# Optimization experiments

Hardware: AMD Instinct MI355X
Metric: run time of the kernel (lower is better)

## Reference

```python
import jax, jax.numpy as jnp
import numpy as np

N = 4096          # nodes
IN_DIM = 256
OUT_DIM = 128
EDGE_DIM = 64
N_SAMPLE = 128
N_EDGES = 65536   # undirected edges (edge ids 1..N_EDGES; id 0 = no edge)
ALPHA = 0.2       # leaky-relu negative slope


def _glorot(key, shape):
    fan_in, fan_out = shape[0], shape[-1]
    scale = 1.414 * np.sqrt(2.0 / (fan_in + fan_out))
    return jax.random.normal(key, shape, jnp.float32) * scale


def setup_inputs() -> dict:
    rng = np.random.default_rng(0)
    # sample unique undirected edges (i < j); np.unique sorts lexicographically,
    # which matches torch's row-major e_index.nonzero() ordering, so assigning
    # sequential ids 1..n here makes edges == arange(1, n+1) in the update step.
    ii = rng.integers(0, N, size=3 * N_EDGES)
    jj = rng.integers(0, N, size=3 * N_EDGES)
    lo, hi = np.minimum(ii, jj), np.maximum(ii, jj)
    ok = lo < hi
    pairs = np.unique(np.stack([lo[ok], hi[ok]], axis=1), axis=0)[:N_EDGES]
    n = pairs.shape[0]
    ids = np.arange(1, n + 1, dtype=np.int32)
    e_index = np.zeros((N, N), np.int32)
    e_index[pairs[:, 0], pairs[:, 1]] = ids
    e_index[pairs[:, 1], pairs[:, 0]] = ids
    # per-node neighbor sampling with replacement (hoisted from torch forward)
    neigh = np.empty((N, N_SAMPLE), np.int32)
    for v in range(N):
        nz = np.nonzero(e_index[v])[0]
        neigh[v] = v if nz.size == 0 else rng.choice(nz, N_SAMPLE)

    key = jax.random.key(0)
    ks = jax.random.split(key, 8)
    return {
        "features": jax.random.normal(ks[0], (N, IN_DIM), jnp.float32),
        "e_index": jnp.asarray(e_index),
        "neigh": jnp.asarray(neigh),
        "to_update": jnp.asarray(pairs.astype(np.int32)),
        "emb": jax.random.normal(ks[1], (n + 1, EDGE_DIM), jnp.float32),
        "W": _glorot(ks[2], (IN_DIM, OUT_DIM)),
        "W2": _glorot(ks[3], (OUT_DIM, EDGE_DIM)),
        "W3": _glorot(ks[4], (EDGE_DIM, EDGE_DIM)),
        "B": _glorot(ks[5], (1, EDGE_DIM)),
        "a": _glorot(ks[6], (2 * OUT_DIM + EDGE_DIM, 1)),
    }


def reference(features, e_index, neigh, to_update, emb, W, W2, W3, B, a):
    x = features @ W                                        # [N, OUT]
    xn = x[neigh]                                           # [N, S, OUT] gather
    eid = jnp.take_along_axis(e_index, neigh, axis=1)       # [N, S] edge ids
    en = emb[eid]                                           # [N, S, ED] gather
    a_input = jnp.concatenate(
        [jnp.broadcast_to(x[:, None, :], xn.shape), xn, en], axis=2
    )                                                       # [N, S, 2*OUT+ED]
    e = jax.nn.leaky_relu((a_input @ a)[..., 0], ALPHA)     # [N, S]
    att = jax.nn.softmax(e, axis=1)                         # dropout = id (eval)
    h_prime = jnp.einsum('ns,nsd->nd', att, xn)             # [N, OUT]
    output = jax.nn.elu(h_prime + x)
    # edge update: (output[i] + output[j]) @ W2 == matmul(output[pair], W2).sum(1)
    edges = e_index[to_update[:, 0], to_update[:, 1]]       # == 1..n
    v_input = (output[to_update[:, 0]] + output[to_update[:, 1]]) @ W2
    e_input = emb[edges] @ W3
    a_in2 = jnp.concatenate([B, e_input + v_input + B], axis=0)  # [n+1, ED]
    emb_new = jax.nn.relu(a_in2 * emb)
    return output, emb_new
```

## Files before the change

kernel.cpp:

```cpp
#include <hip/hip_runtime.h>
#include <hip/hip_bf16.h>

#define N_NODES 4096
#define IN_DIM  256
#define OUT_DIM 128
#define EDGE_DIM 64
#define N_SAMPLE 128

__device__ __forceinline__ float wsum64(float v) {
#pragma unroll
  for (int off = 32; off; off >>= 1) v += __shfl_xor(v, off, 64);
  return v;
}
__device__ __forceinline__ float wmax64(float v) {
#pragma unroll
  for (int off = 32; off; off >>= 1) v = fmaxf(v, __shfl_xor(v, off, 64));
  return v;
}
__device__ __forceinline__ float sum16(float v) {
#pragma unroll
  for (int off = 1; off < 16; off <<= 1) v += __shfl_xor(v, off, 64);
  return v;
}

__global__ void __launch_bounds__(128) k1_gemm_s_kernel(const float* __restrict__ feat,
                                                        const float* __restrict__ W,
                                                        const float* __restrict__ emb,
                                                        const float* __restrict__ a,
                                                        float* __restrict__ x,
                                                        float* __restrict__ s1,
                                                        float* __restrict__ s2,
                                                        float* __restrict__ s3, int rows) {
  const int t  = threadIdx.x;
  const int v0 = blockIdx.x * 8;
  __shared__ float f[8][IN_DIM];
  __shared__ float redA[16], redB[16];
  {
    float4* f4 = reinterpret_cast<float4*>(&f[0][0]);
    const float4* g4 = reinterpret_cast<const float4*>(&feat[v0 * IN_DIM]);
#pragma unroll
    for (int i = 0; i < 4; ++i) f4[t + 128 * i] = g4[t + 128 * i];
  }
  __syncthreads();
  float acc[8] = {0.f, 0.f, 0.f, 0.f, 0.f, 0.f, 0.f, 0.f};
#pragma unroll 2
  for (int i = 0; i < IN_DIM; i += 4) {
    const float w0 = W[(i + 0) * OUT_DIM + t];
    const float w1 = W[(i + 1) * OUT_DIM + t];
    const float w2 = W[(i + 2) * OUT_DIM + t];
    const float w3 = W[(i + 3) * OUT_DIM + t];
#pragma unroll
    for (int r = 0; r < 8; ++r) {
      const float4 fv = *reinterpret_cast<const float4*>(&f[r][i]);
      acc[r] += fv.x * w0 + fv.y * w1 + fv.z * w2 + fv.w * w3;
    }
  }
  const int wv = t >> 6;
  const float a1t = a[t], a2t = a[OUT_DIM + t];
#pragma unroll
  for (int r = 0; r < 8; ++r) {
    x[(v0 + r) * OUT_DIM + t] = acc[r];
    const float q1 = wsum64(acc[r] * a1t);
    const float q2 = wsum64(acc[r] * a2t);
    if ((t & 63) == 0) { redA[wv * 8 + r] = q1; redB[wv * 8 + r] = q2; }
  }
  __syncthreads();
  if (t < 8) {
    s1[v0 + t] = redA[t] + redA[8 + t];
    s2[v0 + t] = redB[t] + redB[8 + t];
  }
  const int gw  = blockIdx.x * 2 + wv;
  const int l   = t & 63;
  const int sub = l >> 4, q = l & 15;
  const float4 a3q = *reinterpret_cast<const float4*>(&a[2 * OUT_DIM + q * 4]);
  for (int r0 = gw * 4; r0 < rows; r0 += 4096) {
    const int r = r0 + sub;
    float v = 0.f;
    if (r < rows) {
      const float4 e4 = *reinterpret_cast<const float4*>(&emb[r * EDGE_DIM + q * 4]);
      v = e4.x * a3q.x + e4.y * a3q.y + e4.z * a3q.z + e4.w * a3q.w;
    }
    v = sum16(v);
    if (q == 0 && r < rows) s3[r] = v;
  }
}

__global__ void __launch_bounds__(256) k2_attn_y_kernel(const float* __restrict__ x,
                                                        const float* __restrict__ s1,
                                                        const float* __restrict__ s2,
                                                        const float* __restrict__ s3,
                                                        const int* __restrict__ neigh,
                                                        const int* __restrict__ eidx,
                                                        const float* __restrict__ W2,
                                                        float* __restrict__ out,
                                                        float* __restrict__ Y) {
  const int v = blockIdx.x;
  const int t = threadIdx.x;
  const int w = t >> 6, l = t & 63;
  __shared__ float attC[N_SAMPLE];
  __shared__ int   usC[N_SAMPLE];
  __shared__ float redC[4];
  __shared__ float4 hpC[8][32];
  __shared__ float orow[OUT_DIM];
  __shared__ float partY[4][EDGE_DIM];

  if (t < N_SAMPLE) {
    const int u = neigh[v * N_SAMPLE + t];
    usC[t] = u;
    float e = s1[v] + s2[u] + s3[eidx[v * N_NODES + u]];
    e = e > 0.f ? e : 0.2f * e;
    attC[t] = e;
    const float m = wmax64(e);
    if (l == 0) redC[w] = m;
  }
  __syncthreads();
  const float m = fmaxf(redC[0], redC[1]);
  if (t < N_SAMPLE) {
    const float p = __expf(attC[t] - m);
    attC[t] = p;
    const float s = wsum64(p);
    if (l == 0) redC[2 + w] = s;
  }
  __syncthreads();
  const float inv = 1.0f / (redC[2] + redC[3]);

  {
    const int half = l >> 5, cq = l & 31;
    float4 h4 = make_float4(0.f, 0.f, 0.f, 0.f);
    const int s0 = w * 32;
#pragma unroll
    for (int it = 0; it < 16; ++it) {
      const int s = s0 + 2 * it + half;
      const float av = attC[s];
      const float4 xv = *reinterpret_cast<const float4*>(&x[usC[s] * OUT_DIM + cq * 4]);
      h4.x += av * xv.x; h4.y += av * xv.y; h4.z += av * xv.z; h4.w += av * xv.w;
    }
    hpC[w * 2 + half][cq] = h4;
  }
  __syncthreads();
  if (t < 32) {
    float4 H = make_float4(0.f, 0.f, 0.f, 0.f);
#pragma unroll
    for (int p = 0; p < 8; ++p) {
      const float4 v4 = hpC[p][t];
      H.x += v4.x; H.y += v4.y; H.z += v4.z; H.w += v4.w;
    }
    const float4 xs = *reinterpret_cast<const float4*>(&x[v * OUT_DIM + t * 4]);
    float o0 = H.x * inv + xs.x, o1 = H.y * inv + xs.y;
    float o2 = H.z * inv + xs.z, o3 = H.w * inv + xs.w;
    o0 = o0 > 0.f ? o0 : expm1f(o0);
    o1 = o1 > 0.f ? o1 : expm1f(o1);
    o2 = o2 > 0.f ? o2 : expm1f(o2);
    o3 = o3 > 0.f ? o3 : expm1f(o3);
    const float4 r = make_float4(o0, o1, o2, o3);
    *reinterpret_cast<float4*>(&out[v * OUT_DIM + t * 4]) = r;
    *reinterpret_cast<float4*>(&orow[t * 4]) = r;
  }
  __syncthreads();

  {
    const int c = t & 63, ks = t >> 6;
    float acc = 0.f;
#pragma unroll 8
    for (int k = ks * 32; k < ks * 32 + 32; ++k)
      acc += orow[k] * W2[k * EDGE_DIM + c];
    partY[ks][c] = acc;
  }
  __syncthreads();
  if (t < EDGE_DIM)
    Y[v * EDGE_DIM + t] = partY[0][t] + partY[1][t] + partY[2][t] + partY[3][t];
}

#define TE 64
__global__ void __launch_bounds__(256) edge_fused_kernel(const float* __restrict__ Y,
                                                         const float* __restrict__ emb,
                                                         const int* __restrict__ eidx,
                                                         const int* __restrict__ tu,
                                                         const float* __restrict__ W3,
                                                         const float* __restrict__ Bv,
                                                         float* __restrict__ emb_new, int n) {
  const int t  = threadIdx.x;
  const int k0 = blockIdx.x * TE;
  __shared__ float Ain[TE][68];
  __shared__ int   tus[2 * TE];

  if (t < 2 * TE) {
    const int idx = 2 * k0 + t;
    tus[t] = (idx < 2 * n) ? tu[idx] : 0;
  }
  {
    const int e  = t >> 2, q = t & 3;
    const int ke = k0 + e;
    if (ke < n) {
      const int i = tu[2 * ke], j = tu[2 * ke + 1];
      const int id = eidx[i * N_NODES + j];
#pragma unroll
      for (int kk = 0; kk < 16; kk += 4) {
        const int k = q * 16 + kk;
        *reinterpret_cast<float4*>(&Ain[e][k]) =
            *reinterpret_cast<const float4*>(&emb[id * EDGE_DIM + k]);
      }
    }
  }
  __syncthreads();

  const int e0 = (t >> 4) * 4;
  const int c0 = (t & 15) * 4;
  const float4 b4 = *reinterpret_cast<const float4*>(&Bv[c0]);
  float4 acc[4];
#pragma unroll
  for (int m = 0; m < 4; ++m) acc[m] = b4;

#pragma unroll 4
  for (int k = 0; k < EDGE_DIM; k += 4) {
    float4 a4[4];
#pragma unroll
    for (int m = 0; m < 4; ++m) a4[m] = *reinterpret_cast<const float4*>(&Ain[e0 + m][k]);
#pragma unroll
    for (int kk = 0; kk < 4; ++kk) {
      const float4 wv = *reinterpret_cast<const float4*>(&W3[(k + kk) * EDGE_DIM + c0]);
#pragma unroll
      for (int m = 0; m < 4; ++m) {
        const float av = reinterpret_cast<const float*>(&a4[m])[kk];
        acc[m].x += av * wv.x; acc[m].y += av * wv.y;
        acc[m].z += av * wv.z; acc[m].w += av * wv.w;
      }
    }
  }

#pragma unroll
  for (int m = 0; m < 4; ++m) {
    const int ke = k0 + e0 + m;
    if (ke < n) {
      const int i = tus[2 * (e0 + m)], j = tus[2 * (e0 + m) + 1];
      const float4 yi = *reinterpret_cast<const float4*>(&Y[i * EDGE_DIM + c0]);
      const float4 yj = *reinterpret_cast<const float4*>(&Y[j * EDGE_DIM + c0]);
      const float4 ek = *reinterpret_cast<const float4*>(&emb[(ke + 1) * EDGE_DIM + c0]);
      float4 r;
      r.x = fmaxf((acc[m].x + yi.x + yj.x) * ek.x, 0.f);
      r.y = fmaxf((acc[m].y + yi.y + yj.y) * ek.y, 0.f);
      r.z = fmaxf((acc[m].z + yi.z + yj.z) * ek.z, 0.f);
      r.w = fmaxf((acc[m].w + yi.w + yj.w) * ek.w, 0.f);
      *reinterpret_cast<float4*>(&emb_new[(ke + 1) * EDGE_DIM + c0]) = r;
    }
  }
  if (blockIdx.x == 0 && t < 16) {
    const int cc = t * 4;
    const float4 b0 = *reinterpret_cast<const float4*>(&Bv[cc]);
    const float4 e0v = *reinterpret_cast<const float4*>(&emb[cc]);
    float4 r;
    r.x = fmaxf(b0.x * e0v.x, 0.f);
    r.y = fmaxf(b0.y * e0v.y, 0.f);
    r.z = fmaxf(b0.z * e0v.z, 0.f);
    r.w = fmaxf(b0.w * e0v.w, 0.f);
    *reinterpret_cast<float4*>(&emb_new[cc]) = r;
  }
}

extern "C" void kernel_launch(void* const* d_in, const int* in_sizes, int n_in,
                              void* d_out, int out_size, void* d_ws, size_t ws_size,
                              hipStream_t stream) {
  const float* feat  = (const float*)d_in[0];
  const int*   eidx  = (const int*)d_in[1];
  const int*   neigh = (const int*)d_in[2];
  const int*   tu    = (const int*)d_in[3];
  const float* emb   = (const float*)d_in[4];
  const float* W     = (const float*)d_in[5];
  const float* W2    = (const float*)d_in[6];
  const float* W3    = (const float*)d_in[7];
  const float* Bv    = (const float*)d_in[8];
  const float* a     = (const float*)d_in[9];
  const int n    = in_sizes[3] / 2;
  const int rows = in_sizes[4] / EDGE_DIM;

  float* x  = (float*)d_ws;
  float* s1 = x + N_NODES * OUT_DIM;
  float* s2 = s1 + N_NODES;
  float* s3 = s2 + N_NODES;
  float* Y  = s3 + 65552;

  float* out_nodes = (float*)d_out;
  float* emb_new   = out_nodes + N_NODES * OUT_DIM;

  hipLaunchKernelGGL(k1_gemm_s_kernel, dim3(N_NODES / 8), dim3(128), 0, stream,
                     feat, W, emb, a, x, s1, s2, s3, rows);
  hipLaunchKernelGGL(k2_attn_y_kernel, dim3(N_NODES), dim3(256), 0, stream,
                     x, s1, s2, s3, neigh, eidx, W2, out_nodes, Y);
  hipLaunchKernelGGL(edge_fused_kernel, dim3((n + TE - 1) / TE), dim3(256), 0, stream,
                     Y, emb, eidx, tu, W3, Bv, emb_new, n);
}
```

Baseline: 181.5 us.

## Store bf16 copy of x for neighbor gather and prefetch edge ids in GEMM kernel

The GEMM kernel now also writes a bf16 (round-to-nearest-even) copy of x, which the attention kernel gathers for the weighted neighbor sum, halving gather bytes. The e_index lookups for sampled neighbors are moved into the GEMM kernel, issued before the matmul so their latency overlaps compute, and the results are stored compactly for the attention kernel. The GEMM block processes 4 rows instead of 8, doubling the grid, and the attention kernel gets an occupancy hint. Using bf16 for the aggregation lowers precision of h_prime and adds extra writes.

Measured after the change: 175.4 us. 1.03x faster.

```diff
diff --git a/kernel.cpp b/kernel.cpp
--- a/kernel.cpp
+++ b/kernel.cpp
@@ -23,26 +23,40 @@
   return v;
 }
 
-__global__ void __launch_bounds__(128) k1_gemm_s_kernel(const float* __restrict__ feat,
-                                                        const float* __restrict__ W,
-                                                        const float* __restrict__ emb,
-                                                        const float* __restrict__ a,
-                                                        float* __restrict__ x,
-                                                        float* __restrict__ s1,
-                                                        float* __restrict__ s2,
-                                                        float* __restrict__ s3, int rows) {
+__global__ void __launch_bounds__(128) k1_kernel(const float* __restrict__ feat,
+                                                 const float* __restrict__ W,
+                                                 const float* __restrict__ emb,
+                                                 const int* __restrict__ eidx,
+                                                 const int* __restrict__ neigh,
+                                                 const float* __restrict__ a,
+                                                 float* __restrict__ x,
+                                                 ushort* __restrict__ xh,
+                                                 float* __restrict__ s1,
+                                                 float* __restrict__ s2,
+                                                 float* __restrict__ s3,
+                                                 int* __restrict__ eid_vs, int rows) {
   const int t  = threadIdx.x;
-  const int v0 = blockIdx.x * 8;
-  __shared__ float f[8][IN_DIM];
-  __shared__ float redA[16], redB[16];
+  const int v0 = blockIdx.x * 4;
+  __shared__ float f[4][IN_DIM];
+  __shared__ float redA[8], redB[8];
+
+  int uq[4];
+#pragma unroll
+  for (int q = 0; q < 4; ++q) uq[q] = neigh[(v0 + q) * N_SAMPLE + t];
+
   {
     float4* f4 = reinterpret_cast<float4*>(&f[0][0]);
     const float4* g4 = reinterpret_cast<const float4*>(&feat[v0 * IN_DIM]);
-#pragma unroll
-    for (int i = 0; i < 4; ++i) f4[t + 128 * i] = g4[t + 128 * i];
-  }
-  __syncthreads();
-  float acc[8] = {0.f, 0.f, 0.f, 0.f, 0.f, 0.f, 0.f, 0.f};
+    f4[t]       = g4[t];
+    f4[t + 128] = g4[t + 128];
+  }
+  __syncthreads();
+
+  int eq[4];
+#pragma unroll
+  for (int q = 0; q < 4; ++q) eq[q] = eidx[(v0 + q) * N_NODES + uq[q]];
+
+  float acc[4] = {0.f, 0.f, 0.f, 0.f};
 #pragma unroll 2
   for (int i = 0; i < IN_DIM; i += 4) {
     const float w0 = W[(i + 0) * OUT_DIM + t];
@@ -50,50 +64,59 @@
     const float w2 = W[(i + 2) * OUT_DIM + t];
     const float w3 = W[(i + 3) * OUT_DIM + t];
 #pragma unroll
-    for (int r = 0; r < 8; ++r) {
+    for (int r = 0; r < 4; ++r) {
       const float4 fv = *reinterpret_cast<const float4*>(&f[r][i]);
       acc[r] += fv.x * w0 + fv.y * w1 + fv.z * w2 + fv.w * w3;
     }
   }
+
+#pragma unroll
+  for (int q = 0; q < 4; ++q) eid_vs[(v0 + q) * N_SAMPLE + t] = eq[q];
+
   const int wv = t >> 6;
   const float a1t = a[t], a2t = a[OUT_DIM + t];
 #pragma unroll
-  for (int r = 0; r < 8; ++r) {
+  for (int r = 0; r < 4; ++r) {
     x[(v0 + r) * OUT_DIM + t] = acc[r];
+    unsigned int ub = __float_as_uint(acc[r]);
+    ub += 0x7FFFu + ((ub >> 16) & 1u);
+    xh[(v0 + r) * OUT_DIM + t] = (ushort)(ub >> 16);
     const float q1 = wsum64(acc[r] * a1t);
     const float q2 = wsum64(acc[r] * a2t);
-    if ((t & 63) == 0) { redA[wv * 8 + r] = q1; redB[wv * 8 + r] = q2; }
-  }
-  __syncthreads();
-  if (t < 8) {
-    s1[v0 + t] = redA[t] + redA[8 + t];
-    s2[v0 + t] = redB[t] + redB[8 + t];
-  }
+    if ((t & 63) == 0) { redA[wv * 4 + r] = q1; redB[wv * 4 + r] = q2; }
+  }
+  __syncthreads();
+  if (t < 4) {
+    s1[v0 + t] = redA[t] + redA[4 + t];
+    s2[v0 + t] = redB[t] + redB[4 + t];
+  }
+
   const int gw  = blockIdx.x * 2 + wv;
   const int l   = t & 63;
-  const int sub = l >> 4, q = l & 15;
-  const float4 a3q = *reinterpret_cast<const float4*>(&a[2 * OUT_DIM + q * 4]);
-  for (int r0 = gw * 4; r0 < rows; r0 += 4096) {
+  const int sub = l >> 4, q16 = l & 15;
+  const float4 a3q = *reinterpret_cast<const float4*>(&a[2 * OUT_DIM + q16 * 4]);
+  for (int r0 = gw * 4; r0 < rows; r0 += 8192) {
     const int r = r0 + sub;
     float v = 0.f;
     if (r < rows) {
-      const float4 e4 = *reinterpret_cast<const float4*>(&emb[r * EDGE_DIM + q * 4]);
+      const float4 e4 = *reinterpret_cast<const float4*>(&emb[r * EDGE_DIM + q16 * 4]);
       v = e4.x * a3q.x + e4.y * a3q.y + e4.z * a3q.z + e4.w * a3q.w;
     }
     v = sum16(v);
-    if (q == 0 && r < rows) s3[r] = v;
-  }
-}
-
-__global__ void __launch_bounds__(256) k2_attn_y_kernel(const float* __restrict__ x,
-                                                        const float* __restrict__ s1,
-                                                        const float* __restrict__ s2,
-                                                        const float* __restrict__ s3,
-                                                        const int* __restrict__ neigh,
-                                                        const int* __restrict__ eidx,
-                                                        const float* __restrict__ W2,
-                                                        float* __restrict__ out,
-                                                        float* __restrict__ Y) {
+    if (q16 == 0 && r < rows) s3[r] = v;
+  }
+}
+
+__global__ void __launch_bounds__(256, 4) k2_attn_y_kernel(const float* __restrict__ x,
+                                                           const ushort* __restrict__ xh,
+                                                           const float* __restrict__ s1,
+                                                           const float* __restrict__ s2,
+                                                           const float* __restrict__ s3,
+                                                           const int* __restrict__ neigh,
+                                                           const int* __restrict__ eid_vs,
+                                                           const float* __restrict__ W2,
+                                                           float* __restrict__ out,
+                                                           float* __restrict__ Y) {
   const int v = blockIdx.x;
   const int t = threadIdx.x;
   const int w = t >> 6, l = t & 63;
@@ -106,8 +129,9 @@
 
   if (t < N_SAMPLE) {
     const int u = neigh[v * N_SAMPLE + t];
+    const int eid = eid_vs[v * N_SAMPLE + t];
     usC[t] = u;
-    float e = s1[v] + s2[u] + s3[eidx[v * N_NODES + u]];
+    float e = s1[v] + s2[u] + s3[eid];
     e = e > 0.f ? e : 0.2f * e;
     attC[t] = e;
     const float m = wmax64(e);
@@ -132,8 +156,11 @@
     for (int it = 0; it < 16; ++it) {
       const int s = s0 + 2 * it + half;
       const float av = attC[s];
-      const float4 xv = *reinterpret_cast<const float4*>(&x[usC[s] * OUT_DIM + cq * 4]);
-      h4.x += av * xv.x; h4.y += av * xv.y; h4.z += av * xv.z; h4.w += av * xv.w;
+      const ushort4 xv = *reinterpret_cast<const ushort4*>(&xh[usC[s] * OUT_DIM + cq * 4]);
+      h4.x += av * __uint_as_float((unsigned int)xv.x << 16);
+      h4.y += av * __uint_as_float((unsigned int)xv.y << 16);
+      h4.z += av * __uint_as_float((unsigned int)xv.z << 16);
+      h4.w += av * __uint_as_float((unsigned int)xv.w << 16);
     }
     hpC[w * 2 + half][cq] = h4;
   }
@@ -273,19 +300,22 @@
   const int n    = in_sizes[3] / 2;
   const int rows = in_sizes[4] / EDGE_DIM;
 
-  float* x  = (float*)d_ws;
-  float* s1 = x + N_NODES * OUT_DIM;
-  float* s2 = s1 + N_NODES;
-  float* s3 = s2 + N_NODES;
-  float* Y  = s3 + 65552;
+  float* ws = (float*)d_ws;
+  float* x      = ws;
+  float* s1     = ws + 524288;
+  float* s2     = ws + 528384;
+  float* s3     = ws + 532480;
+  float* Y      = ws + 598032;
+  ushort* xh    = (ushort*)(ws + 860176);
+  int*  eid_vs  = (int*)(ws + 1122320);
 
   float* out_nodes = (float*)d_out;
   float* emb_new   = out_nodes + N_NODES * OUT_DIM;
 
-  hipLaunchKernelGGL(k1_gemm_s_kernel, dim3(N_NODES / 8), dim3(128), 0, stream,
-                     feat, W, emb, a, x, s1, s2, s3, rows);
+  hipLaunchKernelGGL(k1_kernel, dim3(N_NODES / 4), dim3(128), 0, stream,
+                     feat, W, emb, eidx, neigh, a, x, xh, s1, s2, s3, eid_vs, rows);
   hipLaunchKernelGGL(k2_attn_y_kernel, dim3(N_NODES), dim3(256), 0, stream,
-                     x, s1, s2, s3, neigh, eidx, W2, out_nodes, Y);
+                     x, xh, s1, s2, s3, neigh, eid_vs, W2, out_nodes, Y);
   hipLaunchKernelGGL(edge_fused_kernel, dim3((n + TE - 1) / TE), dim3(256), 0, stream,
                      Y, emb, eidx, tu, W3, Bv, emb_new, n);
 }
```
